# Performance work log

Hardware: AMD Instinct MI355X
Metric: run time of the kernel (lower is better)

## Reference

```python
import math
import jax, jax.numpy as jnp
import numpy as np
from jax import lax

_S = 1.0 / (2.0 * math.sqrt(2.0))  # each tap is (1/2)/sqrt(2)


def _haar(x, axis, high, same):
    """2-tap Haar cross-correlation along `axis`.
    low  = [ 1/2, 1/2]/sqrt(2) -> _S*(a+b)
    high = [-1/2, 1/2]/sqrt(2) -> _S*(b-a)
    same=True replicates torch's even-kernel padding='same': one zero on the RIGHT.
    same=False is valid conv (output length n-1).
    """
    if same:
        pad = [(0, 0)] * x.ndim
        pad[axis] = (0, 1)
        x = jnp.pad(x, pad)
    n = x.shape[axis]
    a = lax.slice_in_dim(x, 0, n - 1, axis=axis)
    b = lax.slice_in_dim(x, 1, n, axis=axis)
    return _S * (b - a) if high else _S * (a + b)


def setup_inputs() -> dict:
    key = jax.random.key(0)
    x = jax.random.normal(key, (2, 3, 16, 256, 256), dtype=jnp.float32)
    return {"x": x}


def reference(x):
    # frames axis (dim 2): padding=0 (valid) in the original -> length f-1
    L = _haar(x, 2, False, False)
    H = _haar(x, 2, True, False)
    # height axis (dim 3): padding='same' (zero on right)
    LL = _haar(L, 3, False, True)
    LH = _haar(L, 3, True, True)
    HL = _haar(H, 3, False, True)
    HH = _haar(H, 3, True, True)
    # width axis (dim 4): padding='same'
    LLL = _haar(LL, 4, False, True)
    LLH = _haar(LL, 4, True, True)
    LHL = _haar(LH, 4, False, True)
    LHH = _haar(LH, 4, True, True)
    HLL = _haar(HL, 4, False, True)
    HLH = _haar(HL, 4, True, True)
    HHL = _haar(HH, 4, False, True)
    HHH = _haar(HH, 4, True, True)
    detail = jnp.concatenate((LLH, LHL, LHH, HLL, HLH, HHL, HHH), axis=2)
    # torch .squeeze(1): only drops channel dim if it is size 1
    if detail.shape[1] == 1:
        detail = jnp.squeeze(detail, axis=1)
    return (LLL, detail)
```

## Files before the change

kernel.cpp:

```cpp
#include <hip/hip_runtime.h>
#include <stdint.h>


static constexpr float S = 0.35355339059327373f;
static constexpr int   PLANE = 256 * 256;
static constexpr size_t LLL_ELEMS = (size_t)6 * 15 * PLANE;

__device__ __forceinline__ float4 pack_lo(const float* A) {
    return make_float4(S * (A[0] + A[1]), S * (A[1] + A[2]),
                       S * (A[2] + A[3]), S * (A[3] + A[4]));
}

__device__ __forceinline__ float4 pack_hi(const float* A) {
    return make_float4(S * (A[1] - A[0]), S * (A[2] - A[1]),
                       S * (A[3] - A[2]), S * (A[4] - A[3]));
}

__global__ __launch_bounds__(256) void haar3d_kernel(const float* __restrict__ x,
                                                     float* __restrict__ out) {
    const int tid  = blockIdx.x * 256 + threadIdx.x;
    const int lane = threadIdx.x & 63;
    const int row  = tid >> 6;
    const int h    = row & 255;
    const int t    = row >> 8;
    const int f    = t % 15;
    const int nc   = t / 15;
    const int w    = lane << 2;

    const float* p00 = x + ((size_t)(nc * 16 + f) * 256 + h) * 256 + w;
    const float4 z4 = make_float4(0.f, 0.f, 0.f, 0.f);
    float4 v00 = *(const float4*)(p00);
    float4 v10 = *(const float4*)(p00 + PLANE);
    float4 v01 = z4, v11 = z4;
    if (h < 255) {
        v01 = *(const float4*)(p00 + 256);
        v11 = *(const float4*)(p00 + PLANE + 256);
    }

    const float x00[4] = {v00.x, v00.y, v00.z, v00.w};
    const float x10[4] = {v10.x, v10.y, v10.z, v10.w};
    const float x01[4] = {v01.x, v01.y, v01.z, v01.w};
    const float x11[4] = {v11.x, v11.y, v11.z, v11.w};

    float LL[5], LH[5], HL[5], HH[5];
#pragma unroll
    for (int j = 0; j < 4; ++j) {
        const float l0 = S * (x00[j] + x10[j]);
        const float l1 = S * (x01[j] + x11[j]);
        const float g0 = S * (x10[j] - x00[j]);
        const float g1 = S * (x11[j] - x01[j]);
        LL[j] = S * (l0 + l1);
        LH[j] = S * (l1 - l0);
        HL[j] = S * (g0 + g1);
        HH[j] = S * (g1 - g0);
    }

    const float nLL = __shfl_down(LL[0], 1);
    const float nLH = __shfl_down(LH[0], 1);
    const float nHL = __shfl_down(HL[0], 1);
    const float nHH = __shfl_down(HH[0], 1);
    const bool last = (lane == 63);
    LL[4] = last ? 0.f : nLL;
    LH[4] = last ? 0.f : nLH;
    HL[4] = last ? 0.f : nHL;
    HH[4] = last ? 0.f : nHH;

    const size_t rowOff = ((size_t)h) * 256 + w;
    float* lllDst = out + ((size_t)(nc * 15 + f)) * PLANE + rowOff;
    *(float4*)lllDst = pack_lo(LL);

    float* dbase = out + LLL_ELEMS +
                   ((size_t)nc * 105 + f) * PLANE + rowOff;
    const size_t kStride = (size_t)15 * PLANE;
    *(float4*)(dbase + 0 * kStride) = pack_hi(LL);
    *(float4*)(dbase + 1 * kStride) = pack_lo(LH);
    *(float4*)(dbase + 2 * kStride) = pack_hi(LH);
    *(float4*)(dbase + 3 * kStride) = pack_lo(HL);
    *(float4*)(dbase + 4 * kStride) = pack_hi(HL);
    *(float4*)(dbase + 5 * kStride) = pack_lo(HH);
    *(float4*)(dbase + 6 * kStride) = pack_hi(HH);
}

extern "C" void kernel_launch(void* const* d_in, const int* in_sizes, int n_in,
                              void* d_out, int out_size, void* d_ws, size_t ws_size,
                              hipStream_t stream) {
    const float* x = (const float*)d_in[0];
    float* out = (float*)d_out;
    haar3d_kernel<<<dim3(5760), dim3(256), 0, stream>>>(x, out);
}
```

Before: 202.7 us.

## Process four rows per wave with row reuse and nontemporal stores

Each wave now computes four consecutive output rows. It loads five input row pairs and reuses the frame-axis low/high values across adjacent rows, where before each row reloaded its neighbour, so input reads drop from about 2x to 1.25x. All output stores become nontemporal to avoid polluting the cache with write-only data. The grid shrinks fourfold, which lowers parallelism and raises per-thread register use.

After: 206.1 us. No clear change (+1.7%).

```diff
diff --git a/kernel.cpp b/kernel.cpp
--- a/kernel.cpp
+++ b/kernel.cpp
@@ -6,79 +6,88 @@
 static constexpr int   PLANE = 256 * 256;
 static constexpr size_t LLL_ELEMS = (size_t)6 * 15 * PLANE;
 
-__device__ __forceinline__ float4 pack_lo(const float* A) {
-    return make_float4(S * (A[0] + A[1]), S * (A[1] + A[2]),
-                       S * (A[2] + A[3]), S * (A[3] + A[4]));
+typedef float fvec4 __attribute__((ext_vector_type(4)));
+
+__device__ __forceinline__ void st_nt(float* p, float a, float b, float c, float d) {
+    fvec4 v = {a, b, c, d};
+    __builtin_nontemporal_store(v, (fvec4*)p);
 }
 
-__device__ __forceinline__ float4 pack_hi(const float* A) {
-    return make_float4(S * (A[1] - A[0]), S * (A[2] - A[1]),
-                       S * (A[3] - A[2]), S * (A[4] - A[3]));
+__device__ __forceinline__ void st_lo(float* p, const float* A) {
+    st_nt(p, S * (A[0] + A[1]), S * (A[1] + A[2]),
+             S * (A[2] + A[3]), S * (A[3] + A[4]));
+}
+
+__device__ __forceinline__ void st_hi(float* p, const float* A) {
+    st_nt(p, S * (A[1] - A[0]), S * (A[2] - A[1]),
+             S * (A[3] - A[2]), S * (A[4] - A[3]));
 }
 
 __global__ __launch_bounds__(256) void haar3d_kernel(const float* __restrict__ x,
                                                      float* __restrict__ out) {
-    const int tid  = blockIdx.x * 256 + threadIdx.x;
+    const int wid  = blockIdx.x * 4 + (threadIdx.x >> 6);
     const int lane = threadIdx.x & 63;
-    const int row  = tid >> 6;
-    const int h    = row & 255;
-    const int t    = row >> 8;
+    const int hq   = wid & 63;
+    const int t    = wid >> 6;
     const int f    = t % 15;
     const int nc   = t / 15;
+    const int h0   = hq << 2;
     const int w    = lane << 2;
 
-    const float* p00 = x + ((size_t)(nc * 16 + f) * 256 + h) * 256 + w;
-    const float4 z4 = make_float4(0.f, 0.f, 0.f, 0.f);
-    float4 v00 = *(const float4*)(p00);
-    float4 v10 = *(const float4*)(p00 + PLANE);
-    float4 v01 = z4, v11 = z4;
-    if (h < 255) {
-        v01 = *(const float4*)(p00 + 256);
-        v11 = *(const float4*)(p00 + PLANE + 256);
+    const float* p0 = x + ((size_t)(nc * 16 + f) * 256 + h0) * 256 + w;
+    const float* p1 = p0 + PLANE;
+    const bool lastTile = (h0 == 252);
+
+    float l[5][4], g[5][4];
+#pragma unroll
+    for (int r = 0; r < 5; ++r) {
+        float4 a = make_float4(0.f, 0.f, 0.f, 0.f);
+        float4 b = a;
+        if (r < 4 || !lastTile) {
+            a = *(const float4*)(p0 + r * 256);
+            b = *(const float4*)(p1 + r * 256);
+        }
+        l[r][0] = S * (a.x + b.x);  g[r][0] = S * (b.x - a.x);
+        l[r][1] = S * (a.y + b.y);  g[r][1] = S * (b.y - a.y);
+        l[r][2] = S * (a.z + b.z);  g[r][2] = S * (b.z - a.z);
+        l[r][3] = S * (a.w + b.w);  g[r][3] = S * (b.w - a.w);
     }
 
-    const float x00[4] = {v00.x, v00.y, v00.z, v00.w};
-    const float x10[4] = {v10.x, v10.y, v10.z, v10.w};
-    const float x01[4] = {v01.x, v01.y, v01.z, v01.w};
-    const float x11[4] = {v11.x, v11.y, v11.z, v11.w};
+    const size_t rowOff = ((size_t)h0) * 256 + w;
+    float* lllDst = out + ((size_t)(nc * 15 + f)) * PLANE + rowOff;
+    float* dbase  = out + LLL_ELEMS + ((size_t)nc * 105 + f) * PLANE + rowOff;
+    const size_t kStride = (size_t)15 * PLANE;
+    const bool last = (lane == 63);
 
-    float LL[5], LH[5], HL[5], HH[5];
 #pragma unroll
-    for (int j = 0; j < 4; ++j) {
-        const float l0 = S * (x00[j] + x10[j]);
-        const float l1 = S * (x01[j] + x11[j]);
-        const float g0 = S * (x10[j] - x00[j]);
-        const float g1 = S * (x11[j] - x01[j]);
-        LL[j] = S * (l0 + l1);
-        LH[j] = S * (l1 - l0);
-        HL[j] = S * (g0 + g1);
-        HH[j] = S * (g1 - g0);
+    for (int r = 0; r < 4; ++r) {
+        float LL[5], LH[5], HL[5], HH[5];
+#pragma unroll
+        for (int j = 0; j < 4; ++j) {
+            LL[j] = S * (l[r][j] + l[r + 1][j]);
+            LH[j] = S * (l[r + 1][j] - l[r][j]);
+            HL[j] = S * (g[r][j] + g[r + 1][j]);
+            HH[j] = S * (g[r + 1][j] - g[r][j]);
+        }
+        const float nLL = __shfl_down(LL[0], 1);
+        const float nLH = __shfl_down(LH[0], 1);
+        const float nHL = __shfl_down(HL[0], 1);
+        const float nHH = __shfl_down(HH[0], 1);
+        LL[4] = last ? 0.f : nLL;
+        LH[4] = last ? 0.f : nLH;
+        HL[4] = last ? 0.f : nHL;
+        HH[4] = last ? 0.f : nHH;
+
+        const size_t ro = (size_t)r * 256;
+        st_lo(lllDst + ro,              LL);
+        st_hi(dbase + 0 * kStride + ro, LL);
+        st_lo(dbase + 1 * kStride + ro, LH);
+        st_hi(dbase + 2 * kStride + ro, LH);
+        st_lo(dbase + 3 * kStride + ro, HL);
+        st_hi(dbase + 4 * kStride + ro, HL);
+        st_lo(dbase + 5 * kStride + ro, HH);
+        st_hi(dbase + 6 * kStride + ro, HH);
     }
-
-    const float nLL = __shfl_down(LL[0], 1);
-    const float nLH = __shfl_down(LH[0], 1);
-    const float nHL = __shfl_down(HL[0], 1);
-    const float nHH = __shfl_down(HH[0], 1);
-    const bool last = (lane == 63);
-    LL[4] = last ? 0.f : nLL;
-    LH[4] = last ? 0.f : nLH;
-    HL[4] = last ? 0.f : nHL;
-    HH[4] = last ? 0.f : nHH;
-
-    const size_t rowOff = ((size_t)h) * 256 + w;
-    float* lllDst = out + ((size_t)(nc * 15 + f)) * PLANE + rowOff;
-    *(float4*)lllDst = pack_lo(LL);
-
-    float* dbase = out + LLL_ELEMS +
-                   ((size_t)nc * 105 + f) * PLANE + rowOff;
-    const size_t kStride = (size_t)15 * PLANE;
-    *(float4*)(dbase + 0 * kStride) = pack_hi(LL);
-    *(float4*)(dbase + 1 * kStride) = pack_lo(LH);
-    *(float4*)(dbase + 2 * kStride) = pack_hi(LH);
-    *(float4*)(dbase + 3 * kStride) = pack_lo(HL);
-    *(float4*)(dbase + 4 * kStride) = pack_hi(HL);
-    *(float4*)(dbase + 5 * kStride) = pack_lo(HH);
-    *(float4*)(dbase + 6 * kStride) = pack_hi(HH);
 }
 
 extern "C" void kernel_launch(void* const* d_in, const int* in_sizes, int n_in,
@@ -86,5 +95,5 @@
                               hipStream_t stream) {
     const float* x = (const float*)d_in[0];
     float* out = (float*)d_out;
-    haar3d_kernel<<<dim3(5760), dim3(256), 0, stream>>>(x, out);
+    haar3d_kernel<<<dim3(1440), dim3(256), 0, stream>>>(x, out);
 }
```
